# Performance work log

Hardware: AMD Instinct MI355X
Metric: run time of the kernel (lower is better)

Reference implementation:

```python
import jax, jax.numpy as jnp
import numpy as np

N4, N3, N2, N1, K = 32768, 65536, 131072, 262144, 16
G = 512


def _w(key, fan_in, fan_out):
    return jax.random.normal(key, (fan_in, fan_out), dtype=jnp.float32) / np.sqrt(fan_in)


def setup_inputs() -> dict:
    key = jax.random.key(0)
    ks = jax.random.split(key, 24)

    def edges(k, n_coarse, n_fine):
        # each fine (output) point gathers from K random coarse (input) points
        src = jax.random.randint(k, (n_fine * K,), 0, n_coarse, dtype=jnp.int32)
        dst = jnp.repeat(jnp.arange(n_fine, dtype=jnp.int32), K)
        return src, dst

    src3, dst3 = edges(ks[0], N4, N3)
    src2, dst2 = edges(ks[1], N3, N2)
    src1, dst1 = edges(ks[2], N2, N1)

    def gidx(k, n):
        return jnp.sort(jax.random.randint(k, (n,), 0, G, dtype=jnp.int32))

    inp = {
        'z_mask': jax.random.normal(ks[3], (N4, 64), dtype=jnp.float32),
        'pos4': jax.random.normal(ks[4], (N4, 3), dtype=jnp.float32),
        'pos3': jax.random.normal(ks[5], (N3, 3), dtype=jnp.float32),
        'pos2': jax.random.normal(ks[6], (N2, 3), dtype=jnp.float32),
        'pos1': jax.random.normal(ks[7], (N1, 3), dtype=jnp.float32),
        'g4': gidx(ks[8], N4), 'g3': gidx(ks[9], N3),
        'g2': gidx(ks[10], N2), 'g1': gidx(ks[11], N1),
        # PointConv MLP params: Linear(c_in+3 -> c_mid), CELU, Linear(c_mid -> c_out), max-aggregate
        'w1a': _w(ks[12], 64 + 3, 64), 'b1a': jnp.zeros((64,), jnp.float32),
        'w1b': _w(ks[13], 64, 32), 'b1b': jnp.zeros((32,), jnp.float32),
        'w2a': _w(ks[14], 32 + 3, 16), 'b2a': jnp.zeros((16,), jnp.float32),
        'w2b': _w(ks[15], 16, 16), 'b2b': jnp.zeros((16,), jnp.float32),
        'w3a': _w(ks[16], 16 + 3, 8), 'b3a': jnp.zeros((8,), jnp.float32),
        'w3b': _w(ks[17], 8, 8), 'b3b': jnp.zeros((8,), jnp.float32),
        'wlin': _w(ks[18], 8, 1), 'blin': jnp.zeros((1,), jnp.float32),
        'src3': src3, 'dst3': dst3,
        'src2': src2, 'dst2': dst2,
        'src1': src1, 'dst1': dst1,
    }
    return inp


def point_conv(x_in, pos_in, pos_out, src, dst, w_a, b_a, w_b, b_b, n_out):
    # gather: per-edge neighbor features + relative positions
    rel = pos_in[src] - pos_out[dst]                      # [E, 3]
    feat = jnp.concatenate([x_in[src], rel], axis=-1)     # [E, c_in+3]
    h = jax.nn.celu(feat @ w_a + b_a)                     # [E, c_mid]
    m = h @ w_b + b_b                                     # [E, c_out]
    # scatter: max-aggregate edge messages onto output points
    return jax.ops.segment_max(m, dst, num_segments=n_out)


def reference(z_mask, pos4, pos3, pos2, pos1, g4, g3, g2, g1,
              w1a, b1a, w1b, b1b, w2a, b2a, w2b, b2b, w3a, b3a, w3b, b3b,
              wlin, blin, src3, dst3, src2, dst2, src1, dst1):
    out = jax.nn.celu(point_conv(z_mask, pos4, pos3, src3, dst3, w1a, b1a, w1b, b1b, N3))
    out = jax.nn.celu(point_conv(out, pos3, pos2, src2, dst2, w2a, b2a, w2b, b2b, N2))
    out = jax.nn.celu(point_conv(out, pos2, pos1, src1, dst1, w3a, b3a, w3b, b3b, N1))
    logits = out @ wlin + blin                            # [N1, 1]
    return jax.nn.log_sigmoid(logits)
```

## Files before the change

### kernel.cpp

```cpp
#include <hip/hip_runtime.h>
#include <hip/hip_fp16.h>
#include <math.h>

#define N4C 32768
#define N3C 65536
#define N2C 131072
#define N1C 262144

typedef _Float16 f16x8 __attribute__((ext_vector_type(8)));
typedef float f32x4 __attribute__((ext_vector_type(4)));
typedef float f32x16 __attribute__((ext_vector_type(16)));

__device__ __forceinline__ f32x4 mfma16(f16x8 a, f16x8 b, f32x4 c) {
  return __builtin_amdgcn_mfma_f32_16x16x32_f16(a, b, c, 0, 0, 0);
}
__device__ __forceinline__ f32x16 mfma32(f16x8 a, f16x8 b, f32x16 c) {
  return __builtin_amdgcn_mfma_f32_32x32x16_f16(a, b, c, 0, 0, 0);
}

__device__ __forceinline__ float celuf(float x) {
  return fmaxf(x, 0.f) + (__expf(fminf(x, 0.f)) - 1.f);
}

__device__ __forceinline__ float logsigf(float x) {
  float e = __expf(-fabsf(x));
  return fminf(x, 0.f) - __logf(1.f + e);
}

__device__ __forceinline__ float max3f(float a, float b, float c) {
  return fmaxf(fmaxf(a, b), c);
}

__device__ __forceinline__ _Float16 exp2_16(_Float16 x) {
  __half h; __builtin_memcpy(&h, &x, 2);
  h = hexp2(h);
  _Float16 r; __builtin_memcpy(&r, &h, 2);
  return r;
}

__device__ __forceinline__ f16x8 celu8p1(f16x8 x) {
  f16x8 z = {};
  f16x8 mx = __builtin_elementwise_max(x, z);
  f16x8 mn = __builtin_elementwise_min(x, z) * (_Float16)1.44269504f;
#pragma unroll
  for (int i = 0; i < 8; ++i) mn[i] = exp2_16(mn[i]);
  return mx + mn;
}

__global__ __launch_bounds__(256) void y4_kernel(
    const float* __restrict__ z, const float* __restrict__ pos4,
    const float* __restrict__ w1a, const float* __restrict__ b1a,
    _Float16* __restrict__ y4) {
  const int lane = threadIdx.x & 63, wid = threadIdx.x >> 6;
  const int col = lane & 15, quad = lane >> 4;
  const int base = (blockIdx.x * 4 + wid) * 16;

  f16x8 Ba[2][4];
#pragma unroll
  for (int c = 0; c < 2; ++c)
#pragma unroll
    for (int t = 0; t < 4; ++t)
#pragma unroll
      for (int j = 0; j < 8; ++j)
        Ba[c][t][j] = (_Float16)w1a[(c * 32 + quad * 8 + j) * 64 + t * 16 + col];

  float wr[3][4];
#pragma unroll
  for (int c = 0; c < 3; ++c)
#pragma unroll
    for (int t = 0; t < 4; ++t)
      wr[c][t] = w1a[(64 + c) * 64 + t * 16 + col];

  float px[4], py[4], pz[4];
#pragma unroll
  for (int r = 0; r < 4; ++r) {
    const int row = base + quad * 4 + r;
    px[r] = pos4[row * 3 + 0];
    py[r] = pos4[row * 3 + 1];
    pz[r] = pos4[row * 3 + 2];
  }

  const float* zr = z + (size_t)(base + col) * 64;
  f16x8 A0, A1;
  {
    float4 f0 = *(const float4*)(zr + quad * 8);
    float4 f1 = *(const float4*)(zr + quad * 8 + 4);
    float4 f2 = *(const float4*)(zr + 32 + quad * 8);
    float4 f3 = *(const float4*)(zr + 32 + quad * 8 + 4);
    A0[0] = (_Float16)f0.x; A0[1] = (_Float16)f0.y; A0[2] = (_Float16)f0.z; A0[3] = (_Float16)f0.w;
    A0[4] = (_Float16)f1.x; A0[5] = (_Float16)f1.y; A0[6] = (_Float16)f1.z; A0[7] = (_Float16)f1.w;
    A1[0] = (_Float16)f2.x; A1[1] = (_Float16)f2.y; A1[2] = (_Float16)f2.z; A1[3] = (_Float16)f2.w;
    A1[4] = (_Float16)f3.x; A1[5] = (_Float16)f3.y; A1[6] = (_Float16)f3.z; A1[7] = (_Float16)f3.w;
  }
#pragma unroll
  for (int t = 0; t < 4; ++t) {
    f32x4 acc = {0.f, 0.f, 0.f, 0.f};
    acc = mfma16(A0, Ba[0][t], acc);
    acc = mfma16(A1, Ba[1][t], acc);
    const float bt = b1a[t * 16 + col];
#pragma unroll
    for (int r = 0; r < 4; ++r) {
      const float posterm =
          px[r] * wr[0][t] + py[r] * wr[1][t] + pz[r] * wr[2][t];
      y4[(size_t)(base + quad * 4 + r) * 64 + t * 16 + col] =
          (_Float16)(acc[r] + bt + posterm);
    }
  }
}

__global__ __launch_bounds__(256) void y3_kernel(
    const _Float16* __restrict__ x3f, const float* __restrict__ pos3,
    const float* __restrict__ w2a, const float* __restrict__ b2a,
    _Float16* __restrict__ y3) {
  const int lane = threadIdx.x & 63, wid = threadIdx.x >> 6;
  const int col = lane & 15, quad = lane >> 4;
  const int base = (blockIdx.x * 4 + wid) * 16;

  f16x8 B;
#pragma unroll
  for (int j = 0; j < 8; ++j) B[j] = (_Float16)w2a[(quad * 8 + j) * 16 + col];

  float wr[3];
#pragma unroll
  for (int c = 0; c < 3; ++c) wr[c] = w2a[(32 + c) * 16 + col];

  float px[4], py[4], pz[4];
#pragma unroll
  for (int r = 0; r < 4; ++r) {
    const int row = base + quad * 4 + r;
    px[r] = pos3[row * 3 + 0];
    py[r] = pos3[row * 3 + 1];
    pz[r] = pos3[row * 3 + 2];
  }

  f16x8 A = *(const f16x8*)(x3f + (size_t)(base + col) * 32 + quad * 8);
  f32x4 d = {0.f, 0.f, 0.f, 0.f};
  d = mfma16(A, B, d);
  const float bt = b2a[col];
#pragma unroll
  for (int r = 0; r < 4; ++r) {
    const float posterm = px[r] * wr[0] + py[r] * wr[1] + pz[r] * wr[2];
    y3[(size_t)(base + quad * 4 + r) * 16 + col] =
        (_Float16)(d[r] + bt + posterm);
  }
}

__global__ __launch_bounds__(256) void y2_kernel(
    const _Float16* __restrict__ x2f, const float* __restrict__ pos2,
    const float* __restrict__ w3a, const float* __restrict__ b3a,
    _Float16* __restrict__ y2) {
  const int lane = threadIdx.x & 63, wid = threadIdx.x >> 6;
  const int col = lane & 15, quad = lane >> 4;
  const int base = (blockIdx.x * 4 + wid) * 16;

  f16x8 B;
#pragma unroll
  for (int j = 0; j < 8; ++j) {
    int k = quad * 8 + j;
    B[j] = (k < 16 && col < 8) ? (_Float16)w3a[k * 8 + col] : (_Float16)0.f;
  }
  f16x8 A = *(const f16x8*)(x2f + (size_t)(base + col) * 16 + (quad & 1) * 8);
  f32x4 d = {0.f, 0.f, 0.f, 0.f};
  d = mfma16(A, B, d);
  if (col < 8) {
    float wr[3];
#pragma unroll
    for (int c = 0; c < 3; ++c) wr[c] = w3a[(16 + c) * 8 + col];
    const float bt = b3a[col];
#pragma unroll
    for (int r = 0; r < 4; ++r) {
      const int row = base + quad * 4 + r;
      const float posterm = pos2[row * 3 + 0] * wr[0] +
                            pos2[row * 3 + 1] * wr[1] +
                            pos2[row * 3 + 2] * wr[2];
      y2[(size_t)row * 8 + col] = (_Float16)(d[r] + bt + posterm);
    }
  }
}

__device__ __forceinline__ void l3_compute(
    int p, f16x8 A0, f16x8 A1, _Float16 q0, _Float16 q1, _Float16 q2,
    const f16x8 W0[3], const f16x8 W1[3], const f16x8 Bb[2][2],
    float biasB0, float biasB1, int lane, int col,
    _Float16* __restrict__ x3f) {
  A0 = celu8p1(A0 - (W0[0] * q0 + W0[1] * q1 + W0[2] * q2));
  A1 = celu8p1(A1 - (W1[0] * q0 + W1[1] * q1 + W1[2] * q2));

  f32x4 e0 = {0.f, 0.f, 0.f, 0.f}, e1 = {0.f, 0.f, 0.f, 0.f};
  e0 = mfma16(A0, Bb[0][0], e0);
  e0 = mfma16(A1, Bb[1][0], e0);
  e1 = mfma16(A0, Bb[0][1], e1);
  e1 = mfma16(A1, Bb[1][1], e1);

  float m0 = fmaxf(max3f(e0[0], e0[1], e0[2]), e0[3]);
  float m1 = fmaxf(max3f(e1[0], e1[1], e1[2]), e1[3]);
  m0 = fmaxf(m0, __shfl_xor(m0, 16, 64));
  m0 = fmaxf(m0, __shfl_xor(m0, 32, 64));
  m1 = fmaxf(m1, __shfl_xor(m1, 16, 64));
  m1 = fmaxf(m1, __shfl_xor(m1, 32, 64));
  if (lane < 16) {
    _Float16* row = x3f + (size_t)p * 32;
    row[col]      = (_Float16)celuf(m0 + biasB0);
    row[16 + col] = (_Float16)celuf(m1 + biasB1);
  }
}

__global__ __launch_bounds__(256) void l3_kernel(
    const _Float16* __restrict__ y4, const float* __restrict__ pos3,
    const int* __restrict__ src3, const float* __restrict__ w1a,
    const float* __restrict__ w1b, const float* __restrict__ b1b,
    _Float16* __restrict__ x3f) {
  const int lane = threadIdx.x & 63, wid = threadIdx.x >> 6;
  const int col = lane & 15, quad = lane >> 4;

  f16x8 Bb[2][2];
#pragma unroll
  for (int c = 0; c < 2; ++c)
#pragma unroll
    for (int t = 0; t < 2; ++t)
#pragma unroll
      for (int j = 0; j < 8; ++j)
        Bb[c][t][j] = (_Float16)w1b[(c * 32 + quad * 8 + j) * 32 + t * 16 + col];
  f16x8 W0[3], W1[3];
#pragma unroll
  for (int c = 0; c < 3; ++c)
#pragma unroll
    for (int j = 0; j < 8; ++j) {
      W0[c][j] = (_Float16)w1a[(64 + c) * 64 + quad * 8 + j];
      W1[c][j] = (_Float16)w1a[(64 + c) * 64 + 32 + quad * 8 + j];
    }
  float s0 = 0.f, s1 = 0.f;
#pragma unroll 4
  for (int k = 0; k < 64; ++k) {
    s0 += w1b[k * 32 + col];
    s1 += w1b[k * 32 + 16 + col];
  }
  const float biasB0 = b1b[col] - s0, biasB1 = b1b[16 + col] - s1;

  const int gwave = blockIdx.x * 4 + wid;
  const int nw = gridDim.x << 2;

#pragma unroll 1
  for (int p = gwave; p < N3C; p += 2 * nw) {
    const int p2 = p + nw;
    const int upa = __builtin_amdgcn_readfirstlane(p);
    const int upb = __builtin_amdgcn_readfirstlane(p2);
    const int sa = src3[p * 16 + col];
    const int sb = src3[p2 * 16 + col];

    f16x8 A0a = *(const f16x8*)(y4 + (size_t)sa * 64 + quad * 8);
    f16x8 A1a = *(const f16x8*)(y4 + (size_t)sa * 64 + 32 + quad * 8);
    f16x8 A0b = *(const f16x8*)(y4 + (size_t)sb * 64 + quad * 8);
    f16x8 A1b = *(const f16x8*)(y4 + (size_t)sb * 64 + 32 + quad * 8);

    const _Float16 qa0 = (_Float16)pos3[upa * 3 + 0];
    const _Float16 qa1 = (_Float16)pos3[upa * 3 + 1];
    const _Float16 qa2 = (_Float16)pos3[upa * 3 + 2];
    const _Float16 qb0 = (_Float16)pos3[upb * 3 + 0];
    const _Float16 qb1 = (_Float16)pos3[upb * 3 + 1];
    const _Float16 qb2 = (_Float16)pos3[upb * 3 + 2];

    l3_compute(p,  A0a, A1a, qa0, qa1, qa2, W0, W1, Bb, biasB0, biasB1,
               lane, col, x3f);
    l3_compute(p2, A0b, A1b, qb0, qb1, qb2, W0, W1, Bb, biasB0, biasB1,
               lane, col, x3f);
  }
}

__device__ __forceinline__ void l2_compute(
    int pr, f16x8 A_in, _Float16 q0, _Float16 q1, _Float16 q2,
    const f16x8 W[3], f16x8 Bb, float biasB, int kh, int n,
    _Float16* __restrict__ x2f) {
  f16x8 A = celu8p1(A_in - (W[0] * q0 + W[1] * q1 + W[2] * q2));
  f32x16 acc = {};
  acc = mfma32(A, Bb, acc);

  float mA = fmaxf(max3f(max3f(acc[0], acc[1], acc[2]),
                         max3f(acc[3], acc[4], acc[5]), acc[6]), acc[7]);
  float mB = fmaxf(max3f(max3f(acc[8], acc[9], acc[10]),
                         max3f(acc[11], acc[12], acc[13]), acc[14]), acc[15]);
  mA = fmaxf(mA, __shfl_xor(mA, 32, 64));
  mB = fmaxf(mB, __shfl_xor(mB, 32, 64));

  if (n < 16) {
    const float m = kh ? mB : mA;
    x2f[(size_t)(2 * pr + kh) * 16 + n] = (_Float16)celuf(m + biasB);
  }
}

__global__ __launch_bounds__(256) void l2_kernel(
    const _Float16* __restrict__ y3, const float* __restrict__ pos2,
    const int* __restrict__ src2, const float* __restrict__ w2a,
    const float* __restrict__ w2b, const float* __restrict__ b2b,
    _Float16* __restrict__ x2f) {
  const int lane = threadIdx.x & 63, wid = threadIdx.x >> 6;
  const int n = lane & 31;
  const int e = lane & 15;
  const int h = (lane >> 4) & 1;
  const int kh = lane >> 5;

  f16x8 Bb;
#pragma unroll
  for (int j = 0; j < 8; ++j)
    Bb[j] = (n < 16) ? (_Float16)w2b[(kh * 8 + j) * 16 + n] : (_Float16)0.f;
  f16x8 W[3];
#pragma unroll
  for (int c = 0; c < 3; ++c)
#pragma unroll
    for (int j = 0; j < 8; ++j)
      W[c][j] = (_Float16)w2a[(32 + c) * 16 + kh * 8 + j];
  float ws = 0.f;
#pragma unroll
  for (int k = 0; k < 16; ++k) ws += w2b[k * 16 + (n & 15)];
  const float biasB = b2b[n & 15] - ws;

  const int gwave = blockIdx.x * 4 + wid;
  const int nw = gridDim.x << 2;

#pragma unroll 1
  for (int pr = gwave; pr < N2C / 2; pr += 2 * nw) {
    const int pr2 = pr + nw;
    const int pa = 2 * pr + h, pb = 2 * pr2 + h;
    const int sa = src2[pa * 16 + e];
    const int sb = src2[pb * 16 + e];

    f16x8 Aa = *(const f16x8*)(y3 + (size_t)sa * 16 + kh * 8);
    f16x8 Ab = *(const f16x8*)(y3 + (size_t)sb * 16 + kh * 8);

    const _Float16 qa0 = (_Float16)pos2[pa * 3 + 0];
    const _Float16 qa1 = (_Float16)pos2[pa * 3 + 1];
    const _Float16 qa2 = (_Float16)pos2[pa * 3 + 2];
    const _Float16 qb0 = (_Float16)pos2[pb * 3 + 0];
    const _Float16 qb1 = (_Float16)pos2[pb * 3 + 1];
    const _Float16 qb2 = (_Float16)pos2[pb * 3 + 2];

    l2_compute(pr,  Aa, qa0, qa1, qa2, W, Bb, biasB, kh, n, x2f);
    l2_compute(pr2, Ab, qb0, qb1, qb2, W, Bb, biasB, kh, n, x2f);
  }
}

__device__ __forceinline__ void l1_compute(
    int pb, f16x8 A_in, _Float16 q0, _Float16 q1, _Float16 q2,
    const f16x8 W[3], f16x8 Bb, float biasB, float wl, float bl, int lane,
    float* __restrict__ out) {
  f16x8 A = celu8p1(A_in - (W[0] * q0 + W[1] * q1 + W[2] * q2));
  f32x16 acc = {};
  acc = mfma32(A, Bb, acc);

  float mA = fmaxf(max3f(max3f(acc[0], acc[1], acc[2]),
                         max3f(acc[3], acc[4], acc[5]), acc[6]), acc[7]);
  float mB = fmaxf(max3f(max3f(acc[8], acc[9], acc[10]),
                         max3f(acc[11], acc[12], acc[13]), acc[14]), acc[15]);
  mA = fmaxf(mA, __shfl_xor(mA, 32, 64));
  mB = fmaxf(mB, __shfl_xor(mB, 32, 64));

  float tA = celuf(mA + biasB) * wl;
  float tB = celuf(mB + biasB) * wl;
  tA += __shfl_xor(tA, 1, 64);
  tA += __shfl_xor(tA, 2, 64);
  tA += __shfl_xor(tA, 4, 64);
  tB += __shfl_xor(tB, 1, 64);
  tB += __shfl_xor(tB, 2, 64);
  tB += __shfl_xor(tB, 4, 64);
  if (lane == 0) {
    float2 o; o.x = logsigf(tA + bl); o.y = logsigf(tB + bl);
    *(float2*)(out + pb) = o;
  } else if (lane == 8) {
    float2 o; o.x = logsigf(tA + bl); o.y = logsigf(tB + bl);
    *(float2*)(out + pb + 2) = o;
  }
}

__global__ __launch_bounds__(256) void l1_kernel(
    const _Float16* __restrict__ y2, const float* __restrict__ pos1,
    const int* __restrict__ src1, const float* __restrict__ w3a,
    const float* __restrict__ w3b, const float* __restrict__ b3b,
    const float* __restrict__ wlin, const float* __restrict__ blin,
    float* __restrict__ out) {
  const int lane = threadIdx.x & 63, wid = threadIdx.x >> 6;
  const int m = lane & 31;
  const int e = lane & 15;
  const int h = (lane >> 4) & 1;
  const int kh = lane >> 5;
  const int g = 2 * kh + h;

  f16x8 Bb;
  const int n = m;
#pragma unroll
  for (int j = 0; j < 8; ++j)
    Bb[j] = (n < 16 && (n >> 3) == kh) ? (_Float16)w3b[j * 8 + (n & 7)]
                                       : (_Float16)0.f;
  f16x8 W[3];
#pragma unroll
  for (int c = 0; c < 3; ++c)
#pragma unroll
    for (int j = 0; j < 8; ++j)
      W[c][j] = (_Float16)w3a[(16 + c) * 8 + j];
  float ws = 0.f;
#pragma unroll
  for (int j = 0; j < 8; ++j) ws += w3b[j * 8 + (n & 7)];
  const float biasB = (n < 16) ? b3b[n & 7] - ws : 0.f;
  const float wl = (n < 16) ? wlin[n & 7] : 0.f;
  const float bl = blin[0];

  const int gwave = blockIdx.x * 4 + wid;
  const int nw = gridDim.x << 2;

#pragma unroll 1
  for (int q = gwave; q < N1C / 4; q += 2 * nw) {
    const int q2 = q + nw;
    const int pba = q * 4, pbb = q2 * 4;
    const int pa = pba + g, pb = pbb + g;
    const int sa = src1[pa * 16 + e];
    const int sb = src1[pb * 16 + e];

    f16x8 Aa = *(const f16x8*)(y2 + (size_t)sa * 8);
    f16x8 Ab = *(const f16x8*)(y2 + (size_t)sb * 8);

    const _Float16 qa0 = (_Float16)(pos1[pa * 3 + 0]);
    const _Float16 qa1 = (_Float16)(pos1[pa * 3 + 1]);
    const _Float16 qa2 = (_Float16)(pos1[pa * 3 + 2]);
    const _Float16 qb0 = (_Float16)(pos1[pb * 3 + 0]);
    const _Float16 qb1 = (_Float16)(pos1[pb * 3 + 1]);
    const _Float16 qb2 = (_Float16)(pos1[pb * 3 + 2]);

    l1_compute(pba, Aa, qa0, qa1, qa2, W, Bb, biasB, wl, bl, lane, out);
    l1_compute(pbb, Ab, qb0, qb1, qb2, W, Bb, biasB, wl, bl, lane, out);
  }
}

extern "C" void kernel_launch(void* const* d_in, const int* in_sizes, int n_in,
                              void* d_out, int out_size, void* d_ws, size_t ws_size,
                              hipStream_t stream) {
  const float* z_mask = (const float*)d_in[0];
  const float* pos4 = (const float*)d_in[1];
  const float* pos3 = (const float*)d_in[2];
  const float* pos2 = (const float*)d_in[3];
  const float* pos1 = (const float*)d_in[4];
  const float* w1a = (const float*)d_in[9];
  const float* b1a = (const float*)d_in[10];
  const float* w1b = (const float*)d_in[11];
  const float* b1b = (const float*)d_in[12];
  const float* w2a = (const float*)d_in[13];
  const float* b2a = (const float*)d_in[14];
  const float* w2b = (const float*)d_in[15];
  const float* b2b = (const float*)d_in[16];
  const float* w3a = (const float*)d_in[17];
  const float* b3a = (const float*)d_in[18];
  const float* w3b = (const float*)d_in[19];
  const float* b3b = (const float*)d_in[20];
  const float* wlin = (const float*)d_in[21];
  const float* blin = (const float*)d_in[22];
  const int* src3 = (const int*)d_in[23];
  const int* src2 = (const int*)d_in[25];
  const int* src1 = (const int*)d_in[27];

  char* w = (char*)d_ws;
  _Float16* y4  = (_Float16*)(w);
  _Float16* x3f = (_Float16*)(w + (4u << 20));
  _Float16* y3  = (_Float16*)(w + (8u << 20));
  _Float16* x2f = (_Float16*)(w + (10u << 20));
  _Float16* y2  = (_Float16*)(w + (14u << 20));
  float* out = (float*)d_out;

  y4_kernel<<<512, 256, 0, stream>>>(z_mask, pos4, w1a, b1a, y4);
  l3_kernel<<<2048, 256, 0, stream>>>(y4, pos3, src3, w1a, w1b, b1b, x3f);
  y3_kernel<<<1024, 256, 0, stream>>>(x3f, pos3, w2a, b2a, y3);
  l2_kernel<<<2048, 256, 0, stream>>>(y3, pos2, src2, w2a, w2b, b2b, x2f);
  y2_kernel<<<2048, 256, 0, stream>>>(x2f, pos2, w3a, b3a, y2);
  l1_kernel<<<2048, 256, 0, stream>>>(y2, pos1, src1, w3a, w3b, b3b,
                                      wlin, blin, out);
}
```

Measured before the change: 242.5 us.

## Precompute per-point position projections and restructure l3 around 32x32 MFMA

Extra blocks are added to the dense y3/y2/y4 kernels. They precompute, for every output point, its position times the position rows of the first weight matrix, and store the result as an fp16 table. The gather kernels then subtract a loaded vector instead of redoing the 3-term position FMA for every edge. The l3 kernel is also rewritten to handle two points per wave with a single chain of four 32x32x16 MFMAs, in place of the 16x16 pairs. The workspace layout is reshuffled so the buffers can alias. The change cuts per-edge ALU work and redundant position loads, at the cost of extra memory traffic to write and read the new tables.

```diff
diff --git a/kernel.cpp b/kernel.cpp
--- a/kernel.cpp
+++ b/kernel.cpp
@@ -49,8 +49,25 @@
 
 __global__ __launch_bounds__(256) void y4_kernel(
     const float* __restrict__ z, const float* __restrict__ pos4,
-    const float* __restrict__ w1a, const float* __restrict__ b1a,
-    _Float16* __restrict__ y4) {
+    const float* __restrict__ pos3, const float* __restrict__ w1a,
+    const float* __restrict__ b1a, _Float16* __restrict__ y4,
+    _Float16* __restrict__ vt3) {
+  if (blockIdx.x >= 512) {
+    const int idx = (blockIdx.x - 512) * 256 + threadIdx.x;
+    const int p = idx >> 3, seg = (idx & 7) * 8;
+    const float q0 = pos3[p * 3 + 0];
+    const float q1 = pos3[p * 3 + 1];
+    const float q2 = pos3[p * 3 + 2];
+    f16x8 v;
+#pragma unroll
+    for (int j = 0; j < 8; ++j) {
+      const int k = seg + j;
+      v[j] = (_Float16)(w1a[64 * 64 + k] * q0 + w1a[65 * 64 + k] * q1 +
+                        w1a[66 * 64 + k] * q2);
+    }
+    *(f16x8*)(vt3 + (size_t)p * 64 + seg) = v;
+    return;
+  }
   const int lane = threadIdx.x & 63, wid = threadIdx.x >> 6;
   const int col = lane & 15, quad = lane >> 4;
   const int base = (blockIdx.x * 4 + wid) * 16;
@@ -110,8 +127,25 @@
 
 __global__ __launch_bounds__(256) void y3_kernel(
     const _Float16* __restrict__ x3f, const float* __restrict__ pos3,
-    const float* __restrict__ w2a, const float* __restrict__ b2a,
-    _Float16* __restrict__ y3) {
+    const float* __restrict__ pos2, const float* __restrict__ w2a,
+    const float* __restrict__ b2a, _Float16* __restrict__ y3,
+    _Float16* __restrict__ vt2) {
+  if (blockIdx.x >= 1024) {
+    const int idx = (blockIdx.x - 1024) * 256 + threadIdx.x;
+    const int p = idx >> 1, seg = (idx & 1) * 8;
+    const float q0 = pos2[p * 3 + 0];
+    const float q1 = pos2[p * 3 + 1];
+    const float q2 = pos2[p * 3 + 2];
+    f16x8 v;
+#pragma unroll
+    for (int j = 0; j < 8; ++j) {
+      const int k = seg + j;
+      v[j] = (_Float16)(w2a[32 * 16 + k] * q0 + w2a[33 * 16 + k] * q1 +
+                        w2a[34 * 16 + k] * q2);
+    }
+    *(f16x8*)(vt2 + (size_t)p * 16 + seg) = v;
+    return;
+  }
   const int lane = threadIdx.x & 63, wid = threadIdx.x >> 6;
   const int col = lane & 15, quad = lane >> 4;
   const int base = (blockIdx.x * 4 + wid) * 16;
@@ -147,8 +181,22 @@
 
 __global__ __launch_bounds__(256) void y2_kernel(
     const _Float16* __restrict__ x2f, const float* __restrict__ pos2,
-    const float* __restrict__ w3a, const float* __restrict__ b3a,
-    _Float16* __restrict__ y2) {
+    const float* __restrict__ pos1, const float* __restrict__ w3a,
+    const float* __restrict__ b3a, _Float16* __restrict__ y2,
+    _Float16* __restrict__ vt1) {
+  if (blockIdx.x >= 2048) {
+    const int p = (blockIdx.x - 2048) * 256 + threadIdx.x;
+    const float q0 = pos1[p * 3 + 0];
+    const float q1 = pos1[p * 3 + 1];
+    const float q2 = pos1[p * 3 + 2];
+    f16x8 v;
+#pragma unroll
+    for (int k = 0; k < 8; ++k)
+      v[k] = (_Float16)(w3a[16 * 8 + k] * q0 + w3a[17 * 8 + k] * q1 +
+                        w3a[18 * 8 + k] * q2);
+    *(f16x8*)(vt1 + (size_t)p * 8) = v;
+    return;
+  }
   const int lane = threadIdx.x & 63, wid = threadIdx.x >> 6;
   const int col = lane & 15, quad = lane >> 4;
   const int base = (blockIdx.x * 4 + wid) * 16;
@@ -178,100 +226,64 @@
   }
 }
 
-__device__ __forceinline__ void l3_compute(
-    int p, f16x8 A0, f16x8 A1, _Float16 q0, _Float16 q1, _Float16 q2,
-    const f16x8 W0[3], const f16x8 W1[3], const f16x8 Bb[2][2],
-    float biasB0, float biasB1, int lane, int col,
-    _Float16* __restrict__ x3f) {
-  A0 = celu8p1(A0 - (W0[0] * q0 + W0[1] * q1 + W0[2] * q2));
-  A1 = celu8p1(A1 - (W1[0] * q0 + W1[1] * q1 + W1[2] * q2));
-
-  f32x4 e0 = {0.f, 0.f, 0.f, 0.f}, e1 = {0.f, 0.f, 0.f, 0.f};
-  e0 = mfma16(A0, Bb[0][0], e0);
-  e0 = mfma16(A1, Bb[1][0], e0);
-  e1 = mfma16(A0, Bb[0][1], e1);
-  e1 = mfma16(A1, Bb[1][1], e1);
-
-  float m0 = fmaxf(max3f(e0[0], e0[1], e0[2]), e0[3]);
-  float m1 = fmaxf(max3f(e1[0], e1[1], e1[2]), e1[3]);
-  m0 = fmaxf(m0, __shfl_xor(m0, 16, 64));
-  m0 = fmaxf(m0, __shfl_xor(m0, 32, 64));
-  m1 = fmaxf(m1, __shfl_xor(m1, 16, 64));
-  m1 = fmaxf(m1, __shfl_xor(m1, 32, 64));
-  if (lane < 16) {
-    _Float16* row = x3f + (size_t)p * 32;
-    row[col]      = (_Float16)celuf(m0 + biasB0);
-    row[16 + col] = (_Float16)celuf(m1 + biasB1);
-  }
-}
-
 __global__ __launch_bounds__(256) void l3_kernel(
-    const _Float16* __restrict__ y4, const float* __restrict__ pos3,
-    const int* __restrict__ src3, const float* __restrict__ w1a,
-    const float* __restrict__ w1b, const float* __restrict__ b1b,
-    _Float16* __restrict__ x3f) {
-  const int lane = threadIdx.x & 63, wid = threadIdx.x >> 6;
-  const int col = lane & 15, quad = lane >> 4;
-
-  f16x8 Bb[2][2];
-#pragma unroll
-  for (int c = 0; c < 2; ++c)
-#pragma unroll
-    for (int t = 0; t < 2; ++t)
-#pragma unroll
-      for (int j = 0; j < 8; ++j)
-        Bb[c][t][j] = (_Float16)w1b[(c * 32 + quad * 8 + j) * 32 + t * 16 + col];
-  f16x8 W0[3], W1[3];
-#pragma unroll
-  for (int c = 0; c < 3; ++c)
-#pragma unroll
-    for (int j = 0; j < 8; ++j) {
-      W0[c][j] = (_Float16)w1a[(64 + c) * 64 + quad * 8 + j];
-      W1[c][j] = (_Float16)w1a[(64 + c) * 64 + 32 + quad * 8 + j];
-    }
-  float s0 = 0.f, s1 = 0.f;
+    const _Float16* __restrict__ y4, const _Float16* __restrict__ vt3,
+    const int* __restrict__ src3, const float* __restrict__ w1b,
+    const float* __restrict__ b1b, _Float16* __restrict__ x3f) {
+  const int lane = threadIdx.x & 63, wid = threadIdx.x >> 6;
+  const int n = lane & 31;
+  const int kh = lane >> 5;
+
+  f16x8 Bb[4];
+#pragma unroll
+  for (int ks = 0; ks < 4; ++ks)
+#pragma unroll
+    for (int j = 0; j < 8; ++j)
+      Bb[ks][j] = (_Float16)w1b[(ks * 16 + kh * 8 + j) * 32 + n];
+
+  float s = 0.f;
 #pragma unroll 4
-  for (int k = 0; k < 64; ++k) {
-    s0 += w1b[k * 32 + col];
-    s1 += w1b[k * 32 + 16 + col];
-  }
-  const float biasB0 = b1b[col] - s0, biasB1 = b1b[16 + col] - s1;
+  for (int k = 0; k < 32; ++k) s += w1b[(kh * 32 + k) * 32 + n];
+  s += __shfl_xor(s, 32, 64);
+  const float biasB = b1b[n] - s;
 
   const int gwave = blockIdx.x * 4 + wid;
   const int nw = gridDim.x << 2;
 
 #pragma unroll 1
-  for (int p = gwave; p < N3C; p += 2 * nw) {
-    const int p2 = p + nw;
-    const int upa = __builtin_amdgcn_readfirstlane(p);
-    const int upb = __builtin_amdgcn_readfirstlane(p2);
-    const int sa = src3[p * 16 + col];
-    const int sb = src3[p2 * 16 + col];
-
-    f16x8 A0a = *(const f16x8*)(y4 + (size_t)sa * 64 + quad * 8);
-    f16x8 A1a = *(const f16x8*)(y4 + (size_t)sa * 64 + 32 + quad * 8);
-    f16x8 A0b = *(const f16x8*)(y4 + (size_t)sb * 64 + quad * 8);
-    f16x8 A1b = *(const f16x8*)(y4 + (size_t)sb * 64 + 32 + quad * 8);
-
-    const _Float16 qa0 = (_Float16)pos3[upa * 3 + 0];
-    const _Float16 qa1 = (_Float16)pos3[upa * 3 + 1];
-    const _Float16 qa2 = (_Float16)pos3[upa * 3 + 2];
-    const _Float16 qb0 = (_Float16)pos3[upb * 3 + 0];
-    const _Float16 qb1 = (_Float16)pos3[upb * 3 + 1];
-    const _Float16 qb2 = (_Float16)pos3[upb * 3 + 2];
-
-    l3_compute(p,  A0a, A1a, qa0, qa1, qa2, W0, W1, Bb, biasB0, biasB1,
-               lane, col, x3f);
-    l3_compute(p2, A0b, A1b, qb0, qb1, qb2, W0, W1, Bb, biasB0, biasB1,
-               lane, col, x3f);
+  for (int pb = gwave * 2; pb < N3C; pb += nw * 2) {
+    const int s1 = src3[pb * 16 + n];
+    const int p = pb + (n >> 4);
+    const _Float16* yrow = y4 + (size_t)s1 * 64 + kh * 8;
+    const _Float16* vrow = vt3 + (size_t)p * 64 + kh * 8;
+
+    f16x8 A[4];
+#pragma unroll
+    for (int ks = 0; ks < 4; ++ks)
+      A[ks] = *(const f16x8*)(yrow + ks * 16) - *(const f16x8*)(vrow + ks * 16);
+#pragma unroll
+    for (int ks = 0; ks < 4; ++ks) A[ks] = celu8p1(A[ks]);
+
+    f32x16 acc = {};
+#pragma unroll
+    for (int ks = 0; ks < 4; ++ks) acc = mfma32(A[ks], Bb[ks], acc);
+
+    float mA = fmaxf(max3f(max3f(acc[0], acc[1], acc[2]),
+                           max3f(acc[3], acc[4], acc[5]), acc[6]), acc[7]);
+    float mB = fmaxf(max3f(max3f(acc[8], acc[9], acc[10]),
+                           max3f(acc[11], acc[12], acc[13]), acc[14]), acc[15]);
+    mA = fmaxf(mA, __shfl_xor(mA, 32, 64));
+    mB = fmaxf(mB, __shfl_xor(mB, 32, 64));
+
+    const float mv = kh ? mB : mA;
+    x3f[(size_t)(pb + kh) * 32 + n] = (_Float16)celuf(mv + biasB);
   }
 }
 
 __device__ __forceinline__ void l2_compute(
-    int pr, f16x8 A_in, _Float16 q0, _Float16 q1, _Float16 q2,
-    const f16x8 W[3], f16x8 Bb, float biasB, int kh, int n,
+    int pr, f16x8 A_in, f16x8 vt, f16x8 Bb, float biasB, int kh, int n,
     _Float16* __restrict__ x2f) {
-  f16x8 A = celu8p1(A_in - (W[0] * q0 + W[1] * q1 + W[2] * q2));
+  f16x8 A = celu8p1(A_in - vt);
   f32x16 acc = {};
   acc = mfma32(A, Bb, acc);
 
@@ -289,10 +301,9 @@
 }
 
 __global__ __launch_bounds__(256) void l2_kernel(
-    const _Float16* __restrict__ y3, const float* __restrict__ pos2,
-    const int* __restrict__ src2, const float* __restrict__ w2a,
-    const float* __restrict__ w2b, const float* __restrict__ b2b,
-    _Float16* __restrict__ x2f) {
+    const _Float16* __restrict__ y3, const _Float16* __restrict__ vt2,
+    const int* __restrict__ src2, const float* __restrict__ w2b,
+    const float* __restrict__ b2b, _Float16* __restrict__ x2f) {
   const int lane = threadIdx.x & 63, wid = threadIdx.x >> 6;
   const int n = lane & 31;
   const int e = lane & 15;
@@ -303,12 +314,6 @@
 #pragma unroll
   for (int j = 0; j < 8; ++j)
     Bb[j] = (n < 16) ? (_Float16)w2b[(kh * 8 + j) * 16 + n] : (_Float16)0.f;
-  f16x8 W[3];
-#pragma unroll
-  for (int c = 0; c < 3; ++c)
-#pragma unroll
-    for (int j = 0; j < 8; ++j)
-      W[c][j] = (_Float16)w2a[(32 + c) * 16 + kh * 8 + j];
   float ws = 0.f;
 #pragma unroll
   for (int k = 0; k < 16; ++k) ws += w2b[k * 16 + (n & 15)];
@@ -326,24 +331,18 @@
 
     f16x8 Aa = *(const f16x8*)(y3 + (size_t)sa * 16 + kh * 8);
     f16x8 Ab = *(const f16x8*)(y3 + (size_t)sb * 16 + kh * 8);
-
-    const _Float16 qa0 = (_Float16)pos2[pa * 3 + 0];
-    const _Float16 qa1 = (_Float16)pos2[pa * 3 + 1];
-    const _Float16 qa2 = (_Float16)pos2[pa * 3 + 2];
-    const _Float16 qb0 = (_Float16)pos2[pb * 3 + 0];
-    const _Float16 qb1 = (_Float16)pos2[pb * 3 + 1];
-    const _Float16 qb2 = (_Float16)pos2[pb * 3 + 2];
-
-    l2_compute(pr,  Aa, qa0, qa1, qa2, W, Bb, biasB, kh, n, x2f);
-    l2_compute(pr2, Ab, qb0, qb1, qb2, W, Bb, biasB, kh, n, x2f);
+    f16x8 va = *(const f16x8*)(vt2 + (size_t)pa * 16 + kh * 8);
+    f16x8 vb = *(const f16x8*)(vt2 + (size_t)pb * 16 + kh * 8);
+
+    l2_compute(pr,  Aa, va, Bb, biasB, kh, n, x2f);
+    l2_compute(pr2, Ab, vb, Bb, biasB, kh, n, x2f);
   }
 }
 
 __device__ __forceinline__ void l1_compute(
-    int pb, f16x8 A_in, _Float16 q0, _Float16 q1, _Float16 q2,
-    const f16x8 W[3], f16x8 Bb, float biasB, float wl, float bl, int lane,
-    float* __restrict__ out) {
-  f16x8 A = celu8p1(A_in - (W[0] * q0 + W[1] * q1 + W[2] * q2));
+    int pb, f16x8 A_in, f16x8 vt, f16x8 Bb, float biasB, float wl, float bl,
+    int lane, float* __restrict__ out) {
+  f16x8 A = celu8p1(A_in - vt);
   f32x16 acc = {};
   acc = mfma32(A, Bb, acc);
 
@@ -372,11 +371,10 @@
 }
 
 __global__ __launch_bounds__(256) void l1_kernel(
-    const _Float16* __restrict__ y2, const float* __restrict__ pos1,
-    const int* __restrict__ src1, const float* __restrict__ w3a,
-    const float* __restrict__ w3b, const float* __restrict__ b3b,
-    const float* __restrict__ wlin, const float* __restrict__ blin,
-    float* __restrict__ out) {
+    const _Float16* __restrict__ y2, const _Float16* __restrict__ vt1,
+    const int* __restrict__ src1, const float* __restrict__ w3b,
+    const float* __restrict__ b3b, const float* __restrict__ wlin,
+    const float* __restrict__ blin, float* __restrict__ out) {
   const int lane = threadIdx.x & 63, wid = threadIdx.x >> 6;
   const int m = lane & 31;
   const int e = lane & 15;
@@ -390,12 +388,6 @@
   for (int j = 0; j < 8; ++j)
     Bb[j] = (n < 16 && (n >> 3) == kh) ? (_Float16)w3b[j * 8 + (n & 7)]
                                        : (_Float16)0.f;
-  f16x8 W[3];
-#pragma unroll
-  for (int c = 0; c < 3; ++c)
-#pragma unroll
-    for (int j = 0; j < 8; ++j)
-      W[c][j] = (_Float16)w3a[(16 + c) * 8 + j];
   float ws = 0.f;
 #pragma unroll
   for (int j = 0; j < 8; ++j) ws += w3b[j * 8 + (n & 7)];
@@ -416,16 +408,11 @@
 
     f16x8 Aa = *(const f16x8*)(y2 + (size_t)sa * 8);
     f16x8 Ab = *(const f16x8*)(y2 + (size_t)sb * 8);
-
-    const _Float16 qa0 = (_Float16)(pos1[pa * 3 + 0]);
-    const _Float16 qa1 = (_Float16)(pos1[pa * 3 + 1]);
-    const _Float16 qa2 = (_Float16)(pos1[pa * 3 + 2]);
-    const _Float16 qb0 = (_Float16)(pos1[pb * 3 + 0]);
-    const _Float16 qb1 = (_Float16)(pos1[pb * 3 + 1]);
-    const _Float16 qb2 = (_Float16)(pos1[pb * 3 + 2]);
-
-    l1_compute(pba, Aa, qa0, qa1, qa2, W, Bb, biasB, wl, bl, lane, out);
-    l1_compute(pbb, Ab, qb0, qb1, qb2, W, Bb, biasB, wl, bl, lane, out);
+    f16x8 va = *(const f16x8*)(vt1 + (size_t)pa * 8);
+    f16x8 vb = *(const f16x8*)(vt1 + (size_t)pb * 8);
+
+    l1_compute(pba, Aa, va, Bb, biasB, wl, bl, lane, out);
+    l1_compute(pbb, Ab, vb, Bb, biasB, wl, bl, lane, out);
   }
 }
 
@@ -457,17 +444,20 @@
 
   char* w = (char*)d_ws;
   _Float16* y4  = (_Float16*)(w);
-  _Float16* x3f = (_Float16*)(w + (4u << 20));
-  _Float16* y3  = (_Float16*)(w + (8u << 20));
-  _Float16* x2f = (_Float16*)(w + (10u << 20));
-  _Float16* y2  = (_Float16*)(w + (14u << 20));
+  _Float16* vt3 = (_Float16*)(w + (4u << 20));
+  _Float16* x3f = (_Float16*)(w + (12u << 20));
+  _Float16* y3  = (_Float16*)(w);
+  _Float16* vt2 = (_Float16*)(w + (4u << 20));
+  _Float16* x2f = (_Float16*)(w + (8u << 20));
+  _Float16* y2  = (_Float16*)(w + (2u << 20));
+  _Float16* vt1 = (_Float16*)(w + (12u << 20));
   float* out = (float*)d_out;
 
-  y4_kernel<<<512, 256, 0, stream>>>(z_mask, pos4, w1a, b1a, y4);
-  l3_kernel<<<2048, 256, 0, stream>>>(y4, pos3, src3, w1a, w1b, b1b, x3f);
-  y3_kernel<<<1024, 256, 0, stream>>>(x3f, pos3, w2a, b2a, y3);
-  l2_kernel<<<2048, 256, 0, stream>>>(y3, pos2, src2, w2a, w2b, b2b, x2f);
-  y2_kernel<<<2048, 256, 0, stream>>>(x2f, pos2, w3a, b3a, y2);
-  l1_kernel<<<2048, 256, 0, stream>>>(y2, pos1, src1, w3a, w3b, b3b,
+  y4_kernel<<<2560, 256, 0, stream>>>(z_mask, pos4, pos3, w1a, b1a, y4, vt3);
+  l3_kernel<<<2048, 256, 0, stream>>>(y4, vt3, src3, w1b, b1b, x3f);
+  y3_kernel<<<2048, 256, 0, stream>>>(x3f, pos3, pos2, w2a, b2a, y3, vt2);
+  l2_kernel<<<2048, 256, 0, stream>>>(y3, vt2, src2, w2b, b2b, x2f);
+  y2_kernel<<<3072, 256, 0, stream>>>(x2f, pos2, pos1, w3a, b3a, y2, vt1);
+  l1_kernel<<<2048, 256, 0, stream>>>(y2, vt1, src1, w3b, b3b,
                                       wlin, blin, out);
 }
```

Result: faster. 235.0 us (-3.1%).
